# Optimization experiments

Hardware: AMD Instinct MI355X
Metric: run time of the kernel (lower is better)

Reference implementation:

```python
import jax, jax.numpy as jnp
import numpy as np

D_MODEL = 1024
N_HEADS = 16
D_HEAD = D_MODEL // N_HEADS
LN_EPS = 1e-5


def setup_inputs() -> dict:
    key = jax.random.key(0)
    ks = jax.random.split(key, 8)
    B, T = 4, 2048
    s = 1.0 / np.sqrt(D_MODEL)
    return {
        "encoder_seq": jax.random.normal(ks[0], (B, T, D_MODEL), jnp.float32),
        "decoder_seq": jax.random.normal(ks[1], (B, T, D_MODEL), jnp.float32),
        "Wq": jax.random.normal(ks[2], (D_MODEL, D_MODEL), jnp.float32) * s,
        "bq": jnp.zeros((D_MODEL,), jnp.float32),
        "Wk": jax.random.normal(ks[3], (D_MODEL, D_MODEL), jnp.float32) * s,
        "bk": jnp.zeros((D_MODEL,), jnp.float32),
        "Wv": jax.random.normal(ks[4], (D_MODEL, D_MODEL), jnp.float32) * s,
        "bv": jnp.zeros((D_MODEL,), jnp.float32),
        "ln_gamma": jnp.ones((D_MODEL,), jnp.float32),
        "ln_beta": jnp.zeros((D_MODEL,), jnp.float32),
    }


def layer_norm(x, gamma, beta):
    mu = jnp.mean(x, axis=-1, keepdims=True)
    var = jnp.mean(jnp.square(x - mu), axis=-1, keepdims=True)
    return (x - mu) * jax.lax.rsqrt(var + LN_EPS) * gamma + beta


def reference(encoder_seq, decoder_seq, Wq, bq, Wk, bk, Wv, bv, ln_gamma, ln_beta):
    B, T_dec, _ = decoder_seq.shape
    T_enc = encoder_seq.shape[1]
    # projections (torch Linear: x @ W^T + b)
    q = (decoder_seq @ Wq.T + bq).reshape(B, T_dec, N_HEADS, D_HEAD)
    k = (encoder_seq @ Wk.T + bk).reshape(B, T_enc, N_HEADS, D_HEAD)
    v = (encoder_seq @ Wv.T + bv).reshape(B, T_enc, N_HEADS, D_HEAD)
    scale = 1.0 / np.sqrt(D_HEAD)
    # softmax-free attention: scale*(Q K^T) V == scale * Q (K^T V); avoid [T_dec,T_enc]
    kv = jnp.einsum("bthd,bthe->bhde", k, v)          # [B,H,dh,dh]
    att = jnp.einsum("bqhd,bhde->bqhe", q, kv) * scale  # [B,T_dec,H,dh]
    att = att.reshape(B, T_dec, D_MODEL)
    # dropout is identity in eval mode; residual + LayerNorm
    return layer_norm(att + decoder_seq, ln_gamma, ln_beta)
```

## Files before the change

kernel.cpp:

```cpp
#include <hip/hip_runtime.h>
#include <hip/hip_bf16.h>
#include <stdint.h>
#include <stddef.h>

typedef __attribute__((ext_vector_type(8))) __bf16 bf16x8;
typedef __attribute__((ext_vector_type(4))) float f32x4;

#define DMODEL 1024
#define HEADS  16
#define BATCH  4
#define TSEQ   2048
#define MROWS  (BATCH * TSEQ)
#define NE     (MROWS * DMODEL)
#define NW     (DMODEL * DMODEL)

#define MiB (size_t)1048576
#define QB_OFF   ((size_t)0)
#define KB_OFF   (16 * MiB)
#define VB_OFF   (32 * MiB)
#define ENC_OFF  (48 * MiB)
#define DEC_OFF  (64 * MiB)
#define KVP_OFF  (64 * MiB)
#define WB_OFF   (80 * MiB)
#define KVT_OFF  (86 * MiB)

__global__ __launch_bounds__(256)
void conv_all(const float* __restrict__ enc, const float* __restrict__ dec,
              const float* __restrict__ Wq, const float* __restrict__ Wk,
              const float* __restrict__ Wv,
              __bf16* __restrict__ encB, __bf16* __restrict__ decB,
              __bf16* __restrict__ WB)
{
    const int i = (blockIdx.x * 256 + threadIdx.x) * 8;
    const float* src;
    __bf16* dst;
    int off;
    if (i < NE)            { src = enc; dst = encB; off = i; }
    else if (i < 2 * NE)   { src = dec; dst = decB; off = i - NE; }
    else {
        const int j = i - 2 * NE;
        const int sel = j >> 20;
        off = j & (NW - 1);
        src = (sel == 0) ? Wq : (sel == 1) ? Wk : Wv;
        dst = WB + (size_t)sel * NW;
    }
    f32x4 a = *(const f32x4*)(src + off);
    f32x4 b = *(const f32x4*)(src + off + 4);
    bf16x8 o;
#pragma unroll
    for (int j = 0; j < 4; ++j) { o[j] = (__bf16)a[j]; o[j + 4] = (__bf16)b[j]; }
    *(bf16x8*)(dst + off) = o;
}

__device__ __forceinline__ bf16x8 frag(const __bf16* reg, int rowl, int kh, int g4)
{
    const int slot = ((kh << 2) + g4) ^ (rowl & 7);
    return *(const bf16x8*)(reg + rowl * 64 + slot * 8);
}

__device__ __forceinline__ void stage_half(const __bf16* gbase, int kt,
                                           __bf16* reg, int tid)
{
#pragma unroll
    for (int p = 0; p < 2; ++p) {
        const int c = tid + p * 512;
        const int row = c >> 3, slot = c & 7;
        const __bf16* src = gbase + (size_t)row * DMODEL + kt * 64
                            + ((slot ^ (row & 7)) << 3);
        __builtin_amdgcn_global_load_lds(
            (const __attribute__((address_space(1))) void*)src,
            (__attribute__((address_space(3))) void*)(reg + c * 8), 16, 0, 0);
    }
}

#define BARRIER() do { asm volatile("" ::: "memory"); \
    __builtin_amdgcn_s_barrier(); asm volatile("" ::: "memory"); } while (0)
#define VMW(N) asm volatile("s_waitcnt vmcnt(" #N ")" ::: "memory")

#define PHASE(PAR, MH, NH, STAGE_CODE, WAIT_CODE)                             \
  {                                                                           \
    bf16x8 af[4][2], bfv[2][2];                                               \
    _Pragma("unroll") for (int mf = 0; mf < 4; ++mf)                          \
      _Pragma("unroll") for (int kh = 0; kh < 2; ++kh)                        \
        af[mf][kh] = frag(&ldsA[PAR][MH][0], wm * 64 + mf * 16 + l4, kh, g4); \
    _Pragma("unroll") for (int nf = 0; nf < 2; ++nf)                          \
      _Pragma("unroll") for (int kh = 0; kh < 2; ++kh)                        \
        bfv[nf][kh] = frag(&ldsB[PAR][NH][0], wn * 32 + nf * 16 + l4, kh, g4);\
    STAGE_CODE;                                                               \
    WAIT_CODE;                                                                \
    BARRIER();                                                                \
    __builtin_amdgcn_s_setprio(1);                                            \
    _Pragma("unroll") for (int mf = 0; mf < 4; ++mf)                          \
      _Pragma("unroll") for (int nf = 0; nf < 2; ++nf)                        \
        _Pragma("unroll") for (int kh = 0; kh < 2; ++kh)                      \
          acc[MH][NH][mf][nf] = __builtin_amdgcn_mfma_f32_16x16x32_bf16(      \
              af[mf][kh], bfv[nf][kh], acc[MH][NH][mf][nf], 0, 0, 0);         \
    __builtin_amdgcn_s_setprio(0);                                            \
    BARRIER();                                                                \
  }

__global__ __launch_bounds__(512, 2)
void qkv_gemm(const __bf16* __restrict__ decB, const __bf16* __restrict__ encB,
              const __bf16* __restrict__ WB,
              const float* __restrict__ bq, const float* __restrict__ bk,
              const float* __restrict__ bv,
              __bf16* __restrict__ Qb, __bf16* __restrict__ Kb,
              __bf16* __restrict__ Vb)
{
    __shared__ __align__(16) __bf16 ldsA[2][2][8192];
    __shared__ __align__(16) __bf16 ldsB[2][2][8192];

    const int tid  = threadIdx.x;
    const int lane = tid & 63;
    const int wv   = tid >> 6;
    const int wm   = wv >> 2;
    const int wn   = wv & 3;
    const int l4   = lane & 15;
    const int g4   = lane >> 4;

    const int bid  = blockIdx.x;
    const int slab = bid & 7;
    const int idx  = bid >> 3;
    const int r    = idx >> 2;
    const int sel  = r >> 2;
    const int bn   = r & 3;
    const int bm   = slab * 4 + (idx & 3);

    const __bf16* A    = (sel == 0) ? decB : encB;
    const __bf16* W    = WB + (size_t)sel * NW;
    const float*  bias = (sel == 0) ? bq : (sel == 1) ? bk : bv;
    __bf16*       C    = (sel == 0) ? Qb : (sel == 1) ? Kb : Vb;

    const __bf16* Ab = A + (size_t)(bm * 256) * DMODEL;
    const __bf16* Wb = W + (size_t)(bn * 256) * DMODEL;

    auto stA = [&](int par, int hf, int kt) {
        stage_half(Ab + (size_t)hf * 128 * DMODEL, kt, &ldsA[par][hf][0], tid);
    };
    auto stB = [&](int par, int hf, int kt) {
        stage_half(Wb + (size_t)hf * 128 * DMODEL, kt, &ldsB[par][hf][0], tid);
    };

    f32x4 acc[2][2][4][2] = {};

    stA(0, 0, 0); stA(0, 1, 0); stB(0, 0, 0); stB(0, 1, 0);
    stA(1, 0, 1); stA(1, 1, 1); stB(1, 0, 1); stB(1, 1, 1);
    VMW(0);
    BARRIER();

    for (int i = 0; i < 8; ++i) {
        PHASE(0, 0, 0, { if (i > 0) stA(1, 1, 2 * i + 1); }, {})
        PHASE(0, 0, 1, { if (i > 0) stB(1, 1, 2 * i + 1); }, {})
        PHASE(0, 1, 0, { if (i < 7) stA(0, 0, 2 * i + 2); }, {})
        PHASE(0, 1, 1, { if (i < 7) stB(0, 0, 2 * i + 2); },
                       { if (i < 7) VMW(4); else VMW(0); })
        PHASE(1, 0, 0, { if (i < 7) stA(0, 1, 2 * i + 2); }, {})
        PHASE(1, 0, 1, { if (i < 7) stB(0, 1, 2 * i + 2); }, {})
        PHASE(1, 1, 0, { if (i < 7) stA(1, 0, 2 * i + 3); }, {})
        PHASE(1, 1, 1, { if (i < 7) stB(1, 0, 2 * i + 3); },
                       { if (i < 7) VMW(4); })
    }

#pragma unroll
    for (int mh = 0; mh < 2; ++mh)
#pragma unroll
        for (int nh = 0; nh < 2; ++nh)
#pragma unroll
            for (int mf = 0; mf < 4; ++mf)
#pragma unroll
                for (int nf = 0; nf < 2; ++nf) {
                    const int gm0 = bm * 256 + mh * 128 + wm * 64 + mf * 16 + g4 * 4;
                    const int gn  = bn * 256 + nh * 128 + wn * 32 + nf * 16 + l4;
                    const float bv2 = bias[gn];
#pragma unroll
                    for (int j = 0; j < 4; ++j)
                        C[(size_t)(gm0 + j) * DMODEL + gn] =
                            (__bf16)(acc[mh][nh][mf][nf][j] + bv2);
                }
}

__global__ __launch_bounds__(256)
void kv_mm(const __bf16* __restrict__ Kb, const __bf16* __restrict__ Vb,
           float* __restrict__ kvp)
{
    __shared__ __align__(16) float Ks[128][64];
    __shared__ __align__(16) float Vs[128][64];

    const int tid = threadIdx.x;
    const int bh  = blockIdx.x;
    const int ch  = blockIdx.y;
    const int b   = bh >> 4, h = bh & 15;
    const int w   = tid >> 6, lane = tid & 63;
    const int dg  = (lane >> 3) * 8;
    const int eg  = (lane & 7) * 8;
    const size_t base = (size_t)b * TSEQ + (size_t)ch * 512;

    f32x4 acc[8][2] = {};

    for (int ss = 0; ss < 4; ++ss) {
        __syncthreads();
#pragma unroll
        for (int i = 0; i < 4; ++i) {
            const int e = i * 2048 + tid * 8;
            const int t = e >> 6, d = e & 63;
            bf16x8 k8 = *(const bf16x8*)&Kb[(base + ss * 128 + t) * DMODEL + h * 64 + d];
            bf16x8 v8 = *(const bf16x8*)&Vb[(base + ss * 128 + t) * DMODEL + h * 64 + d];
            f32x4 kf0, kf1, vf0, vf1;
#pragma unroll
            for (int j = 0; j < 4; ++j) {
                kf0[j] = (float)k8[j]; kf1[j] = (float)k8[j + 4];
                vf0[j] = (float)v8[j]; vf1[j] = (float)v8[j + 4];
            }
            *(f32x4*)&Ks[t][d]     = kf0;
            *(f32x4*)&Ks[t][d + 4] = kf1;
            *(f32x4*)&Vs[t][d]     = vf0;
            *(f32x4*)&Vs[t][d + 4] = vf1;
        }
        __syncthreads();

#pragma unroll 4
        for (int tt = 0; tt < 32; ++tt) {
            const int t = w * 32 + tt;
            f32x4 kd0 = *(const f32x4*)&Ks[t][dg];
            f32x4 kd1 = *(const f32x4*)&Ks[t][dg + 4];
            f32x4 ve0 = *(const f32x4*)&Vs[t][eg];
            f32x4 ve1 = *(const f32x4*)&Vs[t][eg + 4];
#pragma unroll
            for (int rr = 0; rr < 8; ++rr) {
                const float kd = (rr < 4) ? kd0[rr] : kd1[rr - 4];
                acc[rr][0] += ve0 * kd;
                acc[rr][1] += ve1 * kd;
            }
        }
    }

    float* o = kvp + ((size_t)(ch * 4 + w) * 64 + bh) * 4096 + (size_t)dg * 64 + eg;
#pragma unroll
    for (int rr = 0; rr < 8; ++rr) {
        *(f32x4*)(o + rr * 64)     = acc[rr][0];
        *(f32x4*)(o + rr * 64 + 4) = acc[rr][1];
    }
}

__global__ __launch_bounds__(256)
void kv_reduce(const float* __restrict__ kvp, __bf16* __restrict__ kvT)
{
    const int idx = blockIdx.x * 256 + threadIdx.x;
    const int bh  = idx >> 12;
    const int rem = idx & 4095;
    const int d = rem >> 6, e = rem & 63;
    float s = 0.f;
#pragma unroll
    for (int c = 0; c < 16; ++c) s += kvp[((size_t)c * 64 + bh) * 4096 + rem];
    kvT[(size_t)bh * 4096 + e * 64 + d] = (__bf16)(s * 0.125f);
}

__global__ __launch_bounds__(256)
void att_ln(const __bf16* __restrict__ Q, const __bf16* __restrict__ kvT,
            const float* __restrict__ dec, const float* __restrict__ gamma,
            const float* __restrict__ beta, float* __restrict__ out)
{
    __shared__ __align__(16) __bf16 att_s[32][1032];

    const int tid  = threadIdx.x;
    const int lane = tid & 63;
    const int w    = tid >> 6;
    const int l4   = lane & 15, g4 = lane >> 4;
    const int t0   = blockIdx.x * 32;
    const int b    = t0 >> 11;

#pragma unroll
    for (int i = 0; i < 4; ++i) {
        const int h = w * 4 + i;
        f32x4 acc[2][4] = {};
#pragma unroll
        for (int kk = 0; kk < 2; ++kk) {
            bf16x8 a0 = *(const bf16x8*)&Q[(size_t)(t0 + l4) * DMODEL + h * 64 + kk * 32 + g4 * 8];
            bf16x8 a1 = *(const bf16x8*)&Q[(size_t)(t0 + 16 + l4) * DMODEL + h * 64 + kk * 32 + g4 * 8];
#pragma unroll
            for (int n = 0; n < 4; ++n) {
                bf16x8 bb = *(const bf16x8*)&kvT[(size_t)(b * 16 + h) * 4096 + (n * 16 + l4) * 64 + kk * 32 + g4 * 8];
                acc[0][n] = __builtin_amdgcn_mfma_f32_16x16x32_bf16(a0, bb, acc[0][n], 0, 0, 0);
                acc[1][n] = __builtin_amdgcn_mfma_f32_16x16x32_bf16(a1, bb, acc[1][n], 0, 0, 0);
            }
        }
#pragma unroll
        for (int m = 0; m < 2; ++m)
#pragma unroll
            for (int n = 0; n < 4; ++n)
#pragma unroll
                for (int j = 0; j < 4; ++j)
                    att_s[m * 16 + g4 * 4 + j][h * 64 + n * 16 + l4] = (__bf16)acc[m][n][j];
    }
    __syncthreads();

    const int rr = tid >> 3, seg = tid & 7;
    const size_t grow = (size_t)t0 + rr;
    float sum = 0.f, ss2 = 0.f;
#pragma unroll
    for (int i = 0; i < 16; ++i) {
        const int c0 = seg * 8 + i * 64;
        bf16x8 av = *(const bf16x8*)&att_s[rr][c0];
        f32x4 d0 = *(const f32x4*)&dec[grow * DMODEL + c0];
        f32x4 d1 = *(const f32x4*)&dec[grow * DMODEL + c0 + 4];
        bf16x8 xs;
#pragma unroll
        for (int j = 0; j < 4; ++j) {
            const float x0 = (float)av[j] + d0[j];
            const float x1 = (float)av[j + 4] + d1[j];
            sum += x0 + x1; ss2 += x0 * x0 + x1 * x1;
            xs[j] = (__bf16)x0; xs[j + 4] = (__bf16)x1;
        }
        *(bf16x8*)&att_s[rr][c0] = xs;
    }
    sum += __shfl_xor(sum, 1); ss2 += __shfl_xor(ss2, 1);
    sum += __shfl_xor(sum, 2); ss2 += __shfl_xor(ss2, 2);
    sum += __shfl_xor(sum, 4); ss2 += __shfl_xor(ss2, 4);
    const float mu   = sum * (1.f / 1024.f);
    const float var  = ss2 * (1.f / 1024.f) - mu * mu;
    const float rstd = rsqrtf(var + 1e-5f);

#pragma unroll
    for (int i = 0; i < 16; ++i) {
        const int c0 = seg * 8 + i * 64;
        bf16x8 xv = *(const bf16x8*)&att_s[rr][c0];
        f32x4 g0 = *(const f32x4*)&gamma[c0];
        f32x4 g1 = *(const f32x4*)&gamma[c0 + 4];
        f32x4 b0 = *(const f32x4*)&beta[c0];
        f32x4 b1 = *(const f32x4*)&beta[c0 + 4];
        f32x4 y0, y1;
#pragma unroll
        for (int j = 0; j < 4; ++j) {
            y0[j] = ((float)xv[j]     - mu) * rstd * g0[j] + b0[j];
            y1[j] = ((float)xv[j + 4] - mu) * rstd * g1[j] + b1[j];
        }
        *(f32x4*)&out[grow * DMODEL + c0]     = y0;
        *(f32x4*)&out[grow * DMODEL + c0 + 4] = y1;
    }
}

extern "C" void kernel_launch(void* const* d_in, const int* in_sizes, int n_in,
                              void* d_out, int out_size, void* d_ws, size_t ws_size,
                              hipStream_t stream)
{
    const float* enc   = (const float*)d_in[0];
    const float* dec   = (const float*)d_in[1];
    const float* Wq    = (const float*)d_in[2];
    const float* bq    = (const float*)d_in[3];
    const float* Wk    = (const float*)d_in[4];
    const float* bk    = (const float*)d_in[5];
    const float* Wv    = (const float*)d_in[6];
    const float* bv    = (const float*)d_in[7];
    const float* gamma = (const float*)d_in[8];
    const float* beta  = (const float*)d_in[9];

    char* ws = (char*)d_ws;
    __bf16* Qb   = (__bf16*)(ws + QB_OFF);
    __bf16* Kb   = (__bf16*)(ws + KB_OFF);
    __bf16* Vb   = (__bf16*)(ws + VB_OFF);
    __bf16* encB = (__bf16*)(ws + ENC_OFF);
    __bf16* decB = (__bf16*)(ws + DEC_OFF);
    float*  kvp  = (float*) (ws + KVP_OFF);
    __bf16* WB   = (__bf16*)(ws + WB_OFF);
    __bf16* kvT  = (__bf16*)(ws + KVT_OFF);

    conv_all<<<9728, 256, 0, stream>>>(enc, dec, Wq, Wk, Wv, encB, decB, WB);
    qkv_gemm<<<384, 512, 0, stream>>>(decB, encB, WB, bq, bk, bv, Qb, Kb, Vb);
    kv_mm<<<dim3(64, 4), 256, 0, stream>>>(Kb, Vb, kvp);
    kv_reduce<<<1024, 256, 0, stream>>>(kvp, kvT);
    att_ln<<<256, 256, 0, stream>>>(Qb, kvT, dec, gamma, beta, (float*)d_out);
}
```

Before: 146.3 us.

## Restructure QKV GEMM main loop into full K-tile phases with fewer barriers

Replaces the eight quarter-tile phases per iteration (each with two barriers) with two full K-tile phases. Each phase loads all A and B fragments for a 64-wide K slice, waits on LDS, issues a barrier, and then restages the whole next tile into the same buffer before running 64 MFMAs. The aim is to cut barrier and wait overhead and give the MFMA stream longer uninterrupted runs. In exchange it needs more fragment registers per phase, which may strain the occupancy target of 2 blocks, and it issues coarser, burstier global loads.

```diff
diff --git a/kernel.cpp b/kernel.cpp
--- a/kernel.cpp
+++ b/kernel.cpp
@@ -73,30 +73,36 @@
     }
 }
 
-#define BARRIER() do { asm volatile("" ::: "memory"); \
-    __builtin_amdgcn_s_barrier(); asm volatile("" ::: "memory"); } while (0)
-#define VMW(N) asm volatile("s_waitcnt vmcnt(" #N ")" ::: "memory")
-
-#define PHASE(PAR, MH, NH, STAGE_CODE, WAIT_CODE)                             \
+#define VMW(N)  asm volatile("s_waitcnt vmcnt(" #N ")" ::: "memory")
+#define LGKM0() asm volatile("s_waitcnt lgkmcnt(0)" ::: "memory")
+
+#define KPHASE(PAR, STAGE_CODE, WAIT_CODE)                                    \
   {                                                                           \
-    bf16x8 af[4][2], bfv[2][2];                                               \
-    _Pragma("unroll") for (int mf = 0; mf < 4; ++mf)                          \
-      _Pragma("unroll") for (int kh = 0; kh < 2; ++kh)                        \
-        af[mf][kh] = frag(&ldsA[PAR][MH][0], wm * 64 + mf * 16 + l4, kh, g4); \
-    _Pragma("unroll") for (int nf = 0; nf < 2; ++nf)                          \
-      _Pragma("unroll") for (int kh = 0; kh < 2; ++kh)                        \
-        bfv[nf][kh] = frag(&ldsB[PAR][NH][0], wn * 32 + nf * 16 + l4, kh, g4);\
-    STAGE_CODE;                                                               \
-    WAIT_CODE;                                                                \
-    BARRIER();                                                                \
-    __builtin_amdgcn_s_setprio(1);                                            \
-    _Pragma("unroll") for (int mf = 0; mf < 4; ++mf)                          \
+    bf16x8 af[2][4][2], bfv[2][2][2];                                         \
+    _Pragma("unroll") for (int mh = 0; mh < 2; ++mh)                          \
+      _Pragma("unroll") for (int mf = 0; mf < 4; ++mf)                        \
+        _Pragma("unroll") for (int kh = 0; kh < 2; ++kh)                      \
+          af[mh][mf][kh] = frag(&ldsA[PAR][mh][0], wm * 64 + mf * 16 + l4, kh, g4); \
+    _Pragma("unroll") for (int nh = 0; nh < 2; ++nh)                          \
       _Pragma("unroll") for (int nf = 0; nf < 2; ++nf)                        \
         _Pragma("unroll") for (int kh = 0; kh < 2; ++kh)                      \
-          acc[MH][NH][mf][nf] = __builtin_amdgcn_mfma_f32_16x16x32_bf16(      \
-              af[mf][kh], bfv[nf][kh], acc[MH][NH][mf][nf], 0, 0, 0);         \
+          bfv[nh][nf][kh] = frag(&ldsB[PAR][nh][0], wn * 32 + nf * 16 + l4, kh, g4); \
+    LGKM0();                                                                  \
+    __builtin_amdgcn_sched_barrier(0);                                        \
+    __builtin_amdgcn_s_barrier();        \
+    STAGE_CODE;                      \
+    __builtin_amdgcn_sched_barrier(0);                                        \
+    __builtin_amdgcn_s_setprio(1);                                            \
+    _Pragma("unroll") for (int mh = 0; mh < 2; ++mh)                          \
+      _Pragma("unroll") for (int nh = 0; nh < 2; ++nh)                        \
+        _Pragma("unroll") for (int mf = 0; mf < 4; ++mf)                      \
+          _Pragma("unroll") for (int nf = 0; nf < 2; ++nf)                    \
+            _Pragma("unroll") for (int kh = 0; kh < 2; ++kh)                  \
+              acc[mh][nh][mf][nf] = __builtin_amdgcn_mfma_f32_16x16x32_bf16(  \
+                  af[mh][mf][kh], bfv[nh][nf][kh], acc[mh][nh][mf][nf], 0, 0, 0); \
     __builtin_amdgcn_s_setprio(0);                                            \
-    BARRIER();                                                                \
+    WAIT_CODE;                                                                \
+    __builtin_amdgcn_s_barrier();    \
   }
 
 __global__ __launch_bounds__(512, 2)
@@ -134,31 +140,25 @@
     const __bf16* Ab = A + (size_t)(bm * 256) * DMODEL;
     const __bf16* Wb = W + (size_t)(bn * 256) * DMODEL;
 
-    auto stA = [&](int par, int hf, int kt) {
-        stage_half(Ab + (size_t)hf * 128 * DMODEL, kt, &ldsA[par][hf][0], tid);
+    auto stage_tile = [&](int par, int kt) {
+        stage_half(Ab,                          kt, &ldsA[par][0][0], tid);
+        stage_half(Ab + (size_t)128 * DMODEL,   kt, &ldsA[par][1][0], tid);
+        stage_half(Wb,                          kt, &ldsB[par][0][0], tid);
+        stage_half(Wb + (size_t)128 * DMODEL,   kt, &ldsB[par][1][0], tid);
     };
-    auto stB = [&](int par, int hf, int kt) {
-        stage_half(Wb + (size_t)hf * 128 * DMODEL, kt, &ldsB[par][hf][0], tid);
-    };
 
     f32x4 acc[2][2][4][2] = {};
 
-    stA(0, 0, 0); stA(0, 1, 0); stB(0, 0, 0); stB(0, 1, 0);
-    stA(1, 0, 1); stA(1, 1, 1); stB(1, 0, 1); stB(1, 1, 1);
-    VMW(0);
-    BARRIER();
+    stage_tile(0, 0);
+    stage_tile(1, 1);
+    VMW(8);
+    __builtin_amdgcn_s_barrier();
 
     for (int i = 0; i < 8; ++i) {
-        PHASE(0, 0, 0, { if (i > 0) stA(1, 1, 2 * i + 1); }, {})
-        PHASE(0, 0, 1, { if (i > 0) stB(1, 1, 2 * i + 1); }, {})
-        PHASE(0, 1, 0, { if (i < 7) stA(0, 0, 2 * i + 2); }, {})
-        PHASE(0, 1, 1, { if (i < 7) stB(0, 0, 2 * i + 2); },
-                       { if (i < 7) VMW(4); else VMW(0); })
-        PHASE(1, 0, 0, { if (i < 7) stA(0, 1, 2 * i + 2); }, {})
-        PHASE(1, 0, 1, { if (i < 7) stB(0, 1, 2 * i + 2); }, {})
-        PHASE(1, 1, 0, { if (i < 7) stA(1, 0, 2 * i + 3); }, {})
-        PHASE(1, 1, 1, { if (i < 7) stB(1, 0, 2 * i + 3); },
-                       { if (i < 7) VMW(4); })
+        KPHASE(0, { if (i < 7) stage_tile(0, 2 * i + 2); },
+                  { if (i < 7) { VMW(8); } else { VMW(0); } })
+        KPHASE(1, { if (i < 7) stage_tile(1, 2 * i + 3); },
+                  { if (i < 7) { VMW(8); } else { VMW(0); } })
     }
 
 #pragma unroll
```

Result: faster. 135.3 us (-7.5%).
